# Kernel optimization log

Hardware: AMD Instinct MI355X
Metric: run time of the kernel (lower is better)

The kernel has to match this reference:

```python
import jax, jax.numpy as jnp
import numpy as np

B, N, S, C, H = 16, 64, 4096, 384, 6
DH = C // H
SCALE = DH ** -0.5


def setup_inputs() -> dict:
    k0 = jax.random.key(0)
    ks = jax.random.split(k0, 7)
    std = C ** -0.5
    return {
        "query": jax.random.normal(ks[0], (B, N, C), jnp.float32),
        "key": jax.random.normal(ks[1], (B, S, C), jnp.float32),
        "Wq": jax.random.normal(ks[2], (C, C), jnp.float32) * std,
        "Wk": jax.random.normal(ks[3], (C, C), jnp.float32) * std,
        "Wv": jax.random.normal(ks[4], (C, C), jnp.float32) * std,
        "Wp": jax.random.normal(ks[5], (C, C), jnp.float32) * std,
        "bp": jnp.zeros((C,), jnp.float32),
    }


def reference(query, key, Wq, Wk, Wv, Wp, bp):
    # q/k/v projections (no bias, matching qkv_bias=False); nn.Linear is x @ W.T
    q = (query @ Wq.T).reshape(B, N, H, DH).transpose(0, 2, 1, 3)  # [B,H,N,DH]
    k = (key @ Wk.T).reshape(B, S, H, DH).transpose(0, 2, 1, 3)    # [B,H,S,DH]
    v = (key @ Wv.T).reshape(B, S, H, DH).transpose(0, 2, 1, 3)    # [B,H,S,DH]

    attn = jnp.einsum('bhnd,bhsd->bhns', q, k) * SCALE  # [B,H,N,S]

    # hard_softmax over dim=-2 (the group/query axis): each key token is
    # hard-assigned (straight-through) to its argmax group.
    y_soft = jax.nn.softmax(attn, axis=-2)
    idx = jnp.argmax(y_soft, axis=-2)  # [B,H,S]
    y_hard = (jnp.arange(N)[:, None] == idx[..., None, :]).astype(attn.dtype)  # [B,H,N,S]
    a = y_hard + y_soft - jax.lax.stop_gradient(y_soft)

    # inv_attn renormalization over the key axis
    a = a / (a.sum(axis=-1, keepdims=True) + 1.0)

    out = jnp.einsum('bhns,bhsd->bhnd', a, v)            # [B,H,N,DH]
    out = out.transpose(0, 2, 1, 3).reshape(B, N, C)     # [B,N,C]
    return out @ Wp.T + bp
```

## Files before the change

### kernel.cpp

```cpp
#include <hip/hip_runtime.h>
#include <hip/hip_bf16.h>
#include <stdint.h>

#define B_ 16
#define N_ 64
#define S_ 4096
#define C_ 384
#define H_ 6
#define DH_ 64
#define SCALE_ 0.125f
#define TAU_ 2e-4f
#define LISTCAP 262144

typedef __attribute__((ext_vector_type(8))) short bf16x8;
typedef __attribute__((ext_vector_type(4))) float f32x4;

static __device__ __forceinline__ unsigned short f2bf(float x) {
    union { float f; unsigned u; } v; v.f = x;
    unsigned r = v.u + 0x7FFFu + ((v.u >> 16) & 1u);
    return (unsigned short)(r >> 16);
}
static __device__ __forceinline__ float bf2f(unsigned short b) {
    union { unsigned u; float f; } v; v.u = ((unsigned)b) << 16; return v.f;
}
static __device__ __forceinline__ float bfu_lo(unsigned u) {
    union { unsigned u; float f; } v; v.u = u << 16; return v.f;
}
static __device__ __forceinline__ float bfu_hi(unsigned u) {
    union { unsigned u; float f; } v; v.u = u & 0xFFFF0000u; return v.f;
}

static __device__ __forceinline__ void gl_lds16(const void* g, void* l) {
    __builtin_amdgcn_global_load_lds(
        (const __attribute__((address_space(1))) unsigned int*)g,
        (__attribute__((address_space(3))) unsigned int*)l, 16, 0, 0);
}

#define PREP_BLOCKS 8192
#define QK_BLOCKS   (8 * H_ * B_)

__global__ __launch_bounds__(384) void prepqk_kernel(const float* __restrict__ key,
                                                     unsigned short* __restrict__ khi,
                                                     unsigned short* __restrict__ klo,
                                                     const float* __restrict__ query,
                                                     const float* __restrict__ Wq,
                                                     const float* __restrict__ Wk,
                                                     float* __restrict__ qk,
                                                     unsigned short* __restrict__ qkhi,
                                                     unsigned short* __restrict__ qklo) {
    if (blockIdx.x < PREP_BLOCKS) {
        size_t gid = (size_t)blockIdx.x * 384 + threadIdx.x;
        size_t base = gid * 8;
        float4 x0 = *(const float4*)(key + base);
        float4 x1 = *(const float4*)(key + base + 4);
        float xs[8] = { x0.x, x0.y, x0.z, x0.w, x1.x, x1.y, x1.z, x1.w };
        unsigned short hi[8], lo[8];
#pragma unroll
        for (int i = 0; i < 8; ++i) {
            hi[i] = f2bf(xs[i]);
            lo[i] = f2bf(xs[i] - bf2f(hi[i]));
        }
        *(bf16x8*)(khi + base) = *(bf16x8*)hi;
        *(bf16x8*)(klo + base) = *(bf16x8*)lo;
        return;
    }
    __shared__ float qstage[8][C_];
    __shared__ float qv[8][DH_];
    int e = blockIdx.x - PREP_BLOCKS;
    int ng = e & 7;
    int h = (e >> 3) % H_;
    int b = e / (8 * H_);
    int t = threadIdx.x;
    int n0 = ng * 8;
#pragma unroll
    for (int i = 0; i < 8; ++i)
        qstage[i][t] = query[((size_t)(b * N_ + n0 + i)) * C_ + t];
    __syncthreads();
    if (t < 256) {
        int i0 = t >> 6, d = t & 63;
        const float4* wq = (const float4*)(Wq + (size_t)(h * DH_ + d) * C_);
        float accA = 0.f, accB = 0.f;
#pragma unroll 4
        for (int c4 = 0; c4 < C_ / 4; ++c4) {
            float4 w = wq[c4];
            float4 qa = *(const float4*)&qstage[i0][c4 * 4];
            float4 qb = *(const float4*)&qstage[i0 + 4][c4 * 4];
            accA += qa.x * w.x + qa.y * w.y + qa.z * w.z + qa.w * w.w;
            accB += qb.x * w.x + qb.y * w.y + qb.z * w.z + qb.w * w.w;
        }
        qv[i0][d] = accA * SCALE_;
        qv[i0 + 4][d] = accB * SCALE_;
    }
    __syncthreads();
    float a[8];
#pragma unroll
    for (int i = 0; i < 8; ++i) a[i] = 0.f;
    {
        const float* wk = Wk + (size_t)h * DH_ * C_ + t;
#pragma unroll 4
        for (int d = 0; d < DH_; ++d) {
            float w = wk[(size_t)d * C_];
#pragma unroll
            for (int i = 0; i < 8; ++i) a[i] += qv[i][d] * w;
        }
    }
#pragma unroll
    for (int i = 0; i < 8; ++i) qstage[i][t] = a[i];
    __syncthreads();
    {
        int r = t / 48, c0 = (t % 48) * 8;
        float v[8];
#pragma unroll
        for (int j = 0; j < 8; ++j) v[j] = qstage[r][c0 + j];
        unsigned short hi[8], lo[8];
#pragma unroll
        for (int j = 0; j < 8; ++j) {
            hi[j] = f2bf(v[j]);
            lo[j] = f2bf(v[j] - bf2f(hi[j]));
        }
        size_t o = ((size_t)(b * H_ + h) * N_ + n0 + r) * C_ + c0;
        float4 f0 = { v[0], v[1], v[2], v[3] };
        float4 f1 = { v[4], v[5], v[6], v[7] };
        *(float4*)(qk + o) = f0;
        *(float4*)(qk + o + 4) = f1;
        *(bf16x8*)(qkhi + o) = *(bf16x8*)hi;
        *(bf16x8*)(qklo + o) = *(bf16x8*)lo;
    }
}

__global__ __launch_bounds__(256) void attn_kernel(const unsigned short* __restrict__ qkhi,
                                                   const unsigned short* __restrict__ qklo,
                                                   const unsigned short* __restrict__ khi,
                                                   const unsigned short* __restrict__ klo,
                                                   unsigned int* __restrict__ idx,
                                                   unsigned int* __restrict__ flag_cnt,
                                                   unsigned int* __restrict__ flag_list) {
    __shared__ __align__(16) unsigned short sAhi[64 * 32];
    __shared__ __align__(16) unsigned short sAlo[64 * 32];
    __shared__ __align__(16) unsigned short sBhi[128 * 32];
    __shared__ __align__(16) unsigned short sBlo[128 * 32];
    int tid = threadIdx.x;
    int w = tid >> 6, l = tid & 63;
    int wm = w >> 1, wn = w & 1;
    int q4 = l >> 4, lm = l & 15;
    int s0 = blockIdx.x * 128;
    int h = blockIdx.y, b = blockIdx.z;
    size_t kbK = ((size_t)b * S_ + s0) * C_;
    size_t kbA = (size_t)(b * H_ + h) * N_ * C_;
    int trow16 = l >> 2;
    int tquart = ((l & 3) ^ ((l >> 3) & 3)) * 8;
    int sw = (q4 ^ ((lm >> 1) & 3)) * 8;

    f32x4 acc[2][4];
#pragma unroll
    for (int tm = 0; tm < 2; ++tm)
#pragma unroll
        for (int nt = 0; nt < 4; ++nt) acc[tm][nt] = (f32x4)0.f;

    for (int kc = 0; kc < C_; kc += 32) {
        __syncthreads();
#pragma unroll
        for (int i = 0; i < 6; ++i) {
            int gid = w * 6 + i;
            if (gid < 8) {
                gl_lds16(khi + kbK + (size_t)(gid * 16 + trow16) * C_ + kc + tquart,
                         (char*)sBhi + gid * 1024);
            } else if (gid < 16) {
                int g2 = gid - 8;
                gl_lds16(klo + kbK + (size_t)(g2 * 16 + trow16) * C_ + kc + tquart,
                         (char*)sBlo + g2 * 1024);
            } else if (gid < 20) {
                int g2 = gid - 16;
                gl_lds16(qkhi + kbA + (size_t)(g2 * 16 + trow16) * C_ + kc + tquart,
                         (char*)sAhi + g2 * 1024);
            } else {
                int g2 = gid - 20;
                gl_lds16(qklo + kbA + (size_t)(g2 * 16 + trow16) * C_ + kc + tquart,
                         (char*)sAlo + g2 * 1024);
            }
        }
        __syncthreads();
        bf16x8 ah[2], al[2];
#pragma unroll
        for (int tm = 0; tm < 2; ++tm) {
            int ar = (wm * 32 + tm * 16 + lm) * 32 + sw;
            ah[tm] = *(const bf16x8*)&sAhi[ar];
            al[tm] = *(const bf16x8*)&sAlo[ar];
        }
#pragma unroll
        for (int nt = 0; nt < 4; ++nt) {
            int nr = ((wn * 4 + nt) * 16 + lm) * 32 + sw;
            bf16x8 bh = *(const bf16x8*)&sBhi[nr];
            bf16x8 bl = *(const bf16x8*)&sBlo[nr];
#pragma unroll
            for (int tm = 0; tm < 2; ++tm) {
                acc[tm][nt] = __builtin_amdgcn_mfma_f32_16x16x32_bf16(ah[tm], bh, acc[tm][nt], 0, 0, 0);
                acc[tm][nt] = __builtin_amdgcn_mfma_f32_16x16x32_bf16(ah[tm], bl, acc[tm][nt], 0, 0, 0);
                acc[tm][nt] = __builtin_amdgcn_mfma_f32_16x16x32_bf16(al[tm], bh, acc[tm][nt], 0, 0, 0);
            }
        }
    }
    __syncthreads();

    float* rm1 = (float*)sBhi;
    float* rm2 = rm1 + 256;
    int* ri1 = (int*)(rm2 + 256);
    int* ri2 = ri1 + 256;

#pragma unroll
    for (int nt = 0; nt < 4; ++nt) {
        float m1 = -3.4e38f, m2 = -3.4e38f; int i1 = 0, i2 = 0;
#pragma unroll
        for (int tm = 0; tm < 2; ++tm)
#pragma unroll
            for (int r = 0; r < 4; ++r) {
                float v = acc[tm][nt][r];
                int row = wm * 32 + tm * 16 + q4 * 4 + r;
                if (v > m1) { m2 = m1; i2 = i1; m1 = v; i1 = row; }
                else if (v > m2) { m2 = v; i2 = row; }
            }
#pragma unroll
        for (int off = 16; off < 64; off <<= 1) {
            float om1 = __shfl_xor(m1, off), om2 = __shfl_xor(m2, off);
            int oi1 = __shfl_xor(i1, off), oi2 = __shfl_xor(i2, off);
            bool take = (om1 > m1) || (om1 == m1 && oi1 < i1);
            float w1 = take ? om1 : m1; int wi1 = take ? oi1 : i1;
            float l1 = take ? m1 : om1; int li1 = take ? i1 : oi1;
            float s2 = m2; int si2 = i2;
            if (om2 > s2) { s2 = om2; si2 = oi2; }
            if (l1 > s2) { s2 = l1; si2 = li1; }
            m1 = w1; i1 = wi1; m2 = s2; i2 = si2;
        }
        if (q4 == 0) {
            int cw = (wn * 4 + nt) * 16 + lm;
            rm1[wm * 128 + cw] = m1; rm2[wm * 128 + cw] = m2;
            ri1[wm * 128 + cw] = i1; ri2[wm * 128 + cw] = i2;
        }
    }
    __syncthreads();
    if (tid < 128) {
        float a1 = rm1[tid], a2 = rm2[tid];
        int ai1 = ri1[tid], ai2 = ri2[tid];
        float b1 = rm1[128 + tid], b2 = rm2[128 + tid];
        int bi1 = ri1[128 + tid], bi2 = ri2[128 + tid];
        float w1, s2; int wi1, wi2;
        if (b1 > a1) { w1 = b1; wi1 = bi1; s2 = a1; wi2 = ai1; if (b2 > s2) { s2 = b2; wi2 = bi2; } }
        else         { w1 = a1; wi1 = ai1; s2 = a2; wi2 = ai2; if (b1 > s2) { s2 = b1; wi2 = bi1; } }
        idx[(size_t)(b * H_ + h) * S_ + s0 + tid] = (unsigned)wi1;
        if (w1 - s2 < TAU_) {
            unsigned p = atomicAdd(flag_cnt, 1u);
            if (p < LISTCAP) {
                unsigned tok = (unsigned)((b * H_ + h) * S_ + s0 + tid);
                flag_list[p] = tok | ((unsigned)wi1 << 19) | ((unsigned)wi2 << 25);
            }
        }
    }
}

__global__ __launch_bounds__(256) void fixup_kernel(const float* __restrict__ qk,
                                                    const float* __restrict__ key,
                                                    const unsigned int* __restrict__ flag_list,
                                                    const unsigned int* __restrict__ flag_cnt,
                                                    unsigned int* __restrict__ idx) {
    int w = threadIdx.x >> 6, l = threadIdx.x & 63;
    unsigned total = flag_cnt[0];
    if (total > LISTCAP) total = LISTCAP;
    for (unsigned t = blockIdx.x * 4 + w; t < total; t += gridDim.x * 4) {
        unsigned e = flag_list[t];
        unsigned tok = e & 0x7FFFFu;
        int i1 = (int)((e >> 19) & 63u), i2 = (int)((e >> 25) & 63u);
        unsigned bh = tok >> 12;
        unsigned s = tok & 4095u;
        unsigned bb = bh / H_;
        int l32 = l & 31;
        const float* qrow = qk + ((size_t)bh * N_ + (l < 32 ? i1 : i2)) * C_ + l32 * 12;
        const float* krow = key + ((size_t)bb * S_ + s) * C_ + l32 * 12;
        float sum = 0.f;
#pragma unroll
        for (int c = 0; c < 12; ++c) sum += qrow[c] * krow[c];
#pragma unroll
        for (int off = 1; off < 32; off <<= 1) sum += __shfl_xor(sum, off);
        float d1 = __shfl(sum, 0);
        float d2 = __shfl(sum, 32);
        int win = (d2 > d1 || (d2 == d1 && i2 < i1)) ? i2 : i1;
        if (l == 0) idx[(size_t)bh * S_ + s] = (unsigned)win;
    }
}

__global__ __launch_bounds__(256) void hist_build_kernel(const unsigned int* __restrict__ idx,
                                                         unsigned int* __restrict__ offs,
                                                         unsigned int* __restrict__ order) {
    __shared__ unsigned int cnts[N_];
    __shared__ unsigned int pos[N_];
    int tid = threadIdx.x;
    int bh = blockIdx.x;
    if (tid < N_) cnts[tid] = 0u;
    __syncthreads();
    const unsigned int* idxp = idx + (size_t)bh * S_;
    for (int s = tid; s < S_; s += 256) atomicAdd(&cnts[idxp[s]], 1u);
    __syncthreads();
    if (tid < N_) {
        unsigned v = cnts[tid];
        unsigned x = v;
#pragma unroll
        for (int off = 1; off < 64; off <<= 1) {
            unsigned y = __shfl_up(x, off);
            if (tid >= off) x += y;
        }
        unsigned excl = x - v;
        pos[tid] = excl;
        offs[(size_t)bh * 65 + tid] = excl;
        if (tid == 63) offs[(size_t)bh * 65 + 64] = x;
    }
    __syncthreads();
    unsigned int* op = order + (size_t)bh * S_;
    for (int s = tid; s < S_; s += 256) {
        unsigned g = idxp[s];
        unsigned p = atomicAdd(&pos[g], 1u);
        op[p] = (unsigned)s;
    }
}

#define AGG_PARTS 8
__global__ __launch_bounds__(512) void aggv_kernel(const unsigned short* __restrict__ khi,
                                                   const unsigned int* __restrict__ order,
                                                   const unsigned int* __restrict__ offs,
                                                   const float* __restrict__ Wv,
                                                   float* __restrict__ gvn) {
    __shared__ float lrows[AGG_PARTS][C_];
    int tid = threadIdx.x;
    int part = tid >> 6, l = tid & 63;
    int h = blockIdx.y, b = blockIdx.z;
    int bh = b * H_ + h;
    int g = blockIdx.x;
    unsigned beg = offs[(size_t)bh * 65 + g];
    unsigned end = offs[(size_t)bh * 65 + g + 1];
    int cnt = (int)(end - beg);
    float inv = 1.f / ((float)cnt + 1.f);
    const unsigned int* op = order + (size_t)bh * S_ + beg;
    const unsigned int* kbase = (const unsigned int*)(khi + (size_t)b * S_ * C_);
    float a0 = 0.f, a1 = 0.f, a2 = 0.f, a3 = 0.f, a4 = 0.f, a5 = 0.f;
    for (int base = part * 64; base < cnt; base += 64 * AGG_PARTS) {
        int m = cnt - base; if (m > 64) m = 64;
        unsigned sv = (l < m) ? op[base + l] : 0u;
        int i = 0;
        for (; i + 8 <= m; i += 8) {
            int ss[8];
#pragma unroll
            for (int j = 0; j < 8; ++j) ss[j] = __shfl((int)sv, i + j);
            unsigned u[8][3];
#pragma unroll
            for (int j = 0; j < 8; ++j) {
                const unsigned int* kp = kbase + (size_t)ss[j] * (C_ / 2) + l * 3;
                u[j][0] = kp[0]; u[j][1] = kp[1]; u[j][2] = kp[2];
            }
#pragma unroll
            for (int j = 0; j < 8; ++j) {
                a0 += bfu_lo(u[j][0]); a1 += bfu_hi(u[j][0]);
                a2 += bfu_lo(u[j][1]); a3 += bfu_hi(u[j][1]);
                a4 += bfu_lo(u[j][2]); a5 += bfu_hi(u[j][2]);
            }
        }
        for (; i < m; ++i) {
            int s = (int)__shfl((int)sv, i);
            const unsigned int* kp = kbase + (size_t)s * (C_ / 2) + l * 3;
            unsigned u0 = kp[0], u1 = kp[1], u2 = kp[2];
            a0 += bfu_lo(u0); a1 += bfu_hi(u0);
            a2 += bfu_lo(u1); a3 += bfu_hi(u1);
            a4 += bfu_lo(u2); a5 += bfu_hi(u2);
        }
    }
    float* lp = &lrows[part][l * 6];
    lp[0] = a0 * inv; lp[1] = a1 * inv; lp[2] = a2 * inv;
    lp[3] = a3 * inv; lp[4] = a4 * inv; lp[5] = a5 * inv;
    __syncthreads();
    if (part == 0) {
        const float* wrow = Wv + (size_t)(h * DH_ + l) * C_;
        float acc = 0.f;
#pragma unroll 4
        for (int c4 = 0; c4 < C_ / 4; ++c4) {
            float4 z = *(const float4*)&lrows[0][c4 * 4];
#pragma unroll
            for (int p = 1; p < AGG_PARTS; ++p) {
                float4 y = *(const float4*)&lrows[p][c4 * 4];
                z.x += y.x; z.y += y.y; z.z += y.z; z.w += y.w;
            }
            float4 wv = *(const float4*)&wrow[c4 * 4];
            acc += z.x * wv.x + z.y * wv.y + z.z * wv.z + z.w * wv.w;
        }
        gvn[((size_t)bh * N_ + g) * DH_ + l] = acc;
    }
}

__global__ __launch_bounds__(384) void out_kernel(const float* __restrict__ gvn,
                                                  const float* __restrict__ Wp,
                                                  const float* __restrict__ bp,
                                                  float* __restrict__ out) {
    __shared__ float vals[4][C_];
    int blk = blockIdx.x;
    int b = blk >> 4, n0 = (blk & 15) * 4;
    int t = threadIdx.x;
    int h = t >> 6, d = t & 63;
#pragma unroll
    for (int j = 0; j < 4; ++j)
        vals[j][t] = gvn[((size_t)(b * H_ + h) * N_ + n0 + j) * DH_ + d];
    __syncthreads();
    const float4* w4 = (const float4*)(Wp + (size_t)t * C_);
    float s0 = bp[t], s1 = s0, s2 = s0, s3 = s0;
    const float4* v0 = (const float4*)vals[0];
    const float4* v1 = (const float4*)vals[1];
    const float4* v2 = (const float4*)vals[2];
    const float4* v3 = (const float4*)vals[3];
#pragma unroll 4
    for (int i = 0; i < C_ / 4; ++i) {
        float4 w = w4[i];
        float4 a0 = v0[i]; s0 += a0.x * w.x + a0.y * w.y + a0.z * w.z + a0.w * w.w;
        float4 a1 = v1[i]; s1 += a1.x * w.x + a1.y * w.y + a1.z * w.z + a1.w * w.w;
        float4 a2 = v2[i]; s2 += a2.x * w.x + a2.y * w.y + a2.z * w.z + a2.w * w.w;
        float4 a3 = v3[i]; s3 += a3.x * w.x + a3.y * w.y + a3.z * w.z + a3.w * w.w;
    }
    size_t ob = ((size_t)b * N_ + n0) * C_ + t;
    out[ob] = s0;
    out[ob + C_] = s1;
    out[ob + 2 * C_] = s2;
    out[ob + 3 * C_] = s3;
}

extern "C" void kernel_launch(void* const* d_in, const int* in_sizes, int n_in,
                              void* d_out, int out_size, void* d_ws, size_t ws_size,
                              hipStream_t stream) {
    (void)in_sizes; (void)n_in; (void)out_size; (void)ws_size;
    const float* query = (const float*)d_in[0];
    const float* key   = (const float*)d_in[1];
    const float* Wq    = (const float*)d_in[2];
    const float* Wk    = (const float*)d_in[3];
    const float* Wv    = (const float*)d_in[4];
    const float* Wp    = (const float*)d_in[5];
    const float* bp    = (const float*)d_in[6];
    float* out = (float*)d_out;

    char* ws = (char*)d_ws;
    size_t off = 0;
    unsigned short* khi  = (unsigned short*)(ws + off); off += (size_t)B_ * S_ * C_ * 2;
    unsigned short* klo  = (unsigned short*)(ws + off); off += (size_t)B_ * S_ * C_ * 2;
    float* qk            = (float*)(ws + off);          off += (size_t)B_ * H_ * N_ * C_ * 4;
    unsigned short* qkhi = (unsigned short*)(ws + off); off += (size_t)B_ * H_ * N_ * C_ * 2;
    unsigned short* qklo = (unsigned short*)(ws + off); off += (size_t)B_ * H_ * N_ * C_ * 2;
    unsigned int* idx    = (unsigned int*)(ws + off);   off += (size_t)B_ * H_ * S_ * 4;
    unsigned int* order  = (unsigned int*)(ws + off);   off += (size_t)B_ * H_ * S_ * 4;
    unsigned int* offs   = (unsigned int*)(ws + off);   off += (size_t)B_ * H_ * 65 * 4;
    float* gvn           = (float*)(ws + off);          off += (size_t)B_ * H_ * N_ * DH_ * 4;
    unsigned int* fcnt   = (unsigned int*)(ws + off);   off += 256;
    unsigned int* flist  = (unsigned int*)(ws + off);   off += (size_t)LISTCAP * 4;

    hipMemsetAsync(fcnt, 0, 256, stream);

    prepqk_kernel<<<PREP_BLOCKS + QK_BLOCKS, 384, 0, stream>>>(key, khi, klo,
                                                               query, Wq, Wk, qk, qkhi, qklo);
    attn_kernel<<<dim3(S_ / 128, H_, B_), 256, 0, stream>>>(qkhi, qklo, khi, klo, idx, fcnt, flist);
    fixup_kernel<<<256, 256, 0, stream>>>(qk, key, flist, fcnt, idx);
    hist_build_kernel<<<B_ * H_, 256, 0, stream>>>(idx, offs, order);
    aggv_kernel<<<dim3(N_, H_, B_), 512, 0, stream>>>(khi, order, offs, Wv, gvn);
    out_kernel<<<B_ * N_ / 4, 384, 0, stream>>>(gvn, Wp, bp, out);
}
```

Measured before the change: 449.9 us.

## Transpose Wp/Wv in prep kernel for coalesced weight reads in aggv and out

Adds extra blocks to the prep kernel that transpose Wp and Wv into workspace, so the aggv and out kernels read weights with coalesced column access instead of per-thread strided rows. aggv now reduces partial rows once into shared memory and splits the Wv matvec across all 8 parts. out_kernel runs one block per output row instead of four rows per block. The key bf16 split is also changed to 4-wide accesses. The cost is extra transpose work and writes on every call, plus more blocks and syncs.

```diff
diff --git a/kernel.cpp b/kernel.cpp
--- a/kernel.cpp
+++ b/kernel.cpp
@@ -14,6 +14,7 @@
 
 typedef __attribute__((ext_vector_type(8))) short bf16x8;
 typedef __attribute__((ext_vector_type(4))) float f32x4;
+typedef __attribute__((ext_vector_type(4))) unsigned short u16x4;
 
 static __device__ __forceinline__ unsigned short f2bf(float x) {
     union { float f; unsigned u; } v; v.f = x;
@@ -38,6 +39,7 @@
 
 #define PREP_BLOCKS 8192
 #define QK_BLOCKS   (8 * H_ * B_)
+#define TR_BLOCKS   72
 
 __global__ __launch_bounds__(384) void prepqk_kernel(const float* __restrict__ key,
                                                      unsigned short* __restrict__ khi,
@@ -47,30 +49,62 @@
                                                      const float* __restrict__ Wk,
                                                      float* __restrict__ qk,
                                                      unsigned short* __restrict__ qkhi,
-                                                     unsigned short* __restrict__ qklo) {
-    if (blockIdx.x < PREP_BLOCKS) {
-        size_t gid = (size_t)blockIdx.x * 384 + threadIdx.x;
-        size_t base = gid * 8;
-        float4 x0 = *(const float4*)(key + base);
-        float4 x1 = *(const float4*)(key + base + 4);
-        float xs[8] = { x0.x, x0.y, x0.z, x0.w, x1.x, x1.y, x1.z, x1.w };
-        unsigned short hi[8], lo[8];
-#pragma unroll
-        for (int i = 0; i < 8; ++i) {
-            hi[i] = f2bf(xs[i]);
-            lo[i] = f2bf(xs[i] - bf2f(hi[i]));
-        }
-        *(bf16x8*)(khi + base) = *(bf16x8*)hi;
-        *(bf16x8*)(klo + base) = *(bf16x8*)lo;
-        return;
-    }
+                                                     unsigned short* __restrict__ qklo,
+                                                     const float* __restrict__ Wp,
+                                                     const float* __restrict__ Wv,
+                                                     float* __restrict__ wpT,
+                                                     float* __restrict__ wvT) {
     __shared__ float qstage[8][C_];
     __shared__ float qv[8][DH_];
+    __shared__ float trt[64][65];
+    int t = threadIdx.x;
+    if (blockIdx.x < PREP_BLOCKS) {
+        size_t blk = (size_t)blockIdx.x * 3072;
+#pragma unroll
+        for (int half = 0; half < 2; ++half) {
+            size_t base = blk + (size_t)half * 1536 + (size_t)t * 4;
+            float4 x = *(const float4*)(key + base);
+            float xs[4] = { x.x, x.y, x.z, x.w };
+            unsigned short hi[4], lo[4];
+#pragma unroll
+            for (int i = 0; i < 4; ++i) {
+                hi[i] = f2bf(xs[i]);
+                lo[i] = f2bf(xs[i] - bf2f(hi[i]));
+            }
+            *(u16x4*)(khi + base) = *(u16x4*)hi;
+            *(u16x4*)(klo + base) = *(u16x4*)lo;
+        }
+        return;
+    }
     int e = blockIdx.x - PREP_BLOCKS;
+    if (e >= QK_BLOCKS) {
+        int e2 = e - QK_BLOCKS;
+        const float* src = (e2 < 36) ? Wp : Wv;
+        float* dst = (e2 < 36) ? wpT : wvT;
+        int tile = e2 % 36;
+        int r0 = (tile / 6) * 64, c0 = (tile % 6) * 64;
+        if (t < 256) {
+#pragma unroll
+            for (int rep = 0; rep < 16; ++rep) {
+                int idx = rep * 256 + t;
+                int r = idx >> 6, c = idx & 63;
+                trt[r][c] = src[(size_t)(r0 + r) * C_ + c0 + c];
+            }
+        }
+        __syncthreads();
+        if (t < 256) {
+#pragma unroll
+            for (int rep = 0; rep < 16; ++rep) {
+                int idx = rep * 256 + t;
+                int rT = idx >> 6, cT = idx & 63;
+                dst[(size_t)(c0 + rT) * C_ + r0 + cT] = trt[cT][rT];
+            }
+        }
+        return;
+    }
     int ng = e & 7;
     int h = (e >> 3) % H_;
     int b = e / (8 * H_);
-    int t = threadIdx.x;
     int n0 = ng * 8;
 #pragma unroll
     for (int i = 0; i < 8; ++i)
@@ -325,9 +359,11 @@
 __global__ __launch_bounds__(512) void aggv_kernel(const unsigned short* __restrict__ khi,
                                                    const unsigned int* __restrict__ order,
                                                    const unsigned int* __restrict__ offs,
-                                                   const float* __restrict__ Wv,
+                                                   const float* __restrict__ wvT,
                                                    float* __restrict__ gvn) {
     __shared__ float lrows[AGG_PARTS][C_];
+    __shared__ float zrow[C_];
+    __shared__ float pacc[AGG_PARTS][DH_];
     int tid = threadIdx.x;
     int part = tid >> 6, l = tid & 63;
     int h = blockIdx.y, b = blockIdx.z;
@@ -374,56 +410,48 @@
     lp[0] = a0 * inv; lp[1] = a1 * inv; lp[2] = a2 * inv;
     lp[3] = a3 * inv; lp[4] = a4 * inv; lp[5] = a5 * inv;
     __syncthreads();
+    if (tid < C_) {
+        float z = lrows[0][tid];
+#pragma unroll
+        for (int p = 1; p < AGG_PARTS; ++p) z += lrows[p][tid];
+        zrow[tid] = z;
+    }
+    __syncthreads();
+    {
+        float a = 0.f;
+        int cb = part * (C_ / AGG_PARTS);
+#pragma unroll 8
+        for (int cc = 0; cc < C_ / AGG_PARTS; ++cc) {
+            int c = cb + cc;
+            a += zrow[c] * wvT[(size_t)c * C_ + h * DH_ + l];
+        }
+        pacc[part][l] = a;
+    }
+    __syncthreads();
     if (part == 0) {
-        const float* wrow = Wv + (size_t)(h * DH_ + l) * C_;
-        float acc = 0.f;
-#pragma unroll 4
-        for (int c4 = 0; c4 < C_ / 4; ++c4) {
-            float4 z = *(const float4*)&lrows[0][c4 * 4];
-#pragma unroll
-            for (int p = 1; p < AGG_PARTS; ++p) {
-                float4 y = *(const float4*)&lrows[p][c4 * 4];
-                z.x += y.x; z.y += y.y; z.z += y.z; z.w += y.w;
-            }
-            float4 wv = *(const float4*)&wrow[c4 * 4];
-            acc += z.x * wv.x + z.y * wv.y + z.z * wv.z + z.w * wv.w;
-        }
+        float acc = pacc[0][l];
+#pragma unroll
+        for (int p = 1; p < AGG_PARTS; ++p) acc += pacc[p][l];
         gvn[((size_t)bh * N_ + g) * DH_ + l] = acc;
     }
 }
 
 __global__ __launch_bounds__(384) void out_kernel(const float* __restrict__ gvn,
-                                                  const float* __restrict__ Wp,
+                                                  const float* __restrict__ wpT,
                                                   const float* __restrict__ bp,
                                                   float* __restrict__ out) {
-    __shared__ float vals[4][C_];
-    int blk = blockIdx.x;
-    int b = blk >> 4, n0 = (blk & 15) * 4;
+    __shared__ float vals[C_];
+    int bn = blockIdx.x;
+    int b = bn >> 6, n = bn & 63;
     int t = threadIdx.x;
     int h = t >> 6, d = t & 63;
-#pragma unroll
-    for (int j = 0; j < 4; ++j)
-        vals[j][t] = gvn[((size_t)(b * H_ + h) * N_ + n0 + j) * DH_ + d];
-    __syncthreads();
-    const float4* w4 = (const float4*)(Wp + (size_t)t * C_);
-    float s0 = bp[t], s1 = s0, s2 = s0, s3 = s0;
-    const float4* v0 = (const float4*)vals[0];
-    const float4* v1 = (const float4*)vals[1];
-    const float4* v2 = (const float4*)vals[2];
-    const float4* v3 = (const float4*)vals[3];
-#pragma unroll 4
-    for (int i = 0; i < C_ / 4; ++i) {
-        float4 w = w4[i];
-        float4 a0 = v0[i]; s0 += a0.x * w.x + a0.y * w.y + a0.z * w.z + a0.w * w.w;
-        float4 a1 = v1[i]; s1 += a1.x * w.x + a1.y * w.y + a1.z * w.z + a1.w * w.w;
-        float4 a2 = v2[i]; s2 += a2.x * w.x + a2.y * w.y + a2.z * w.z + a2.w * w.w;
-        float4 a3 = v3[i]; s3 += a3.x * w.x + a3.y * w.y + a3.z * w.z + a3.w * w.w;
-    }
-    size_t ob = ((size_t)b * N_ + n0) * C_ + t;
-    out[ob] = s0;
-    out[ob + C_] = s1;
-    out[ob + 2 * C_] = s2;
-    out[ob + 3 * C_] = s3;
+    vals[t] = gvn[((size_t)(b * H_ + h) * N_ + n) * DH_ + d];
+    __syncthreads();
+    float s = bp[t];
+#pragma unroll 8
+    for (int c = 0; c < C_; ++c)
+        s += vals[c] * wpT[(size_t)c * C_ + t];
+    out[(size_t)bn * C_ + t] = s;
 }
 
 extern "C" void kernel_launch(void* const* d_in, const int* in_sizes, int n_in,
@@ -450,16 +478,18 @@
     unsigned int* order  = (unsigned int*)(ws + off);   off += (size_t)B_ * H_ * S_ * 4;
     unsigned int* offs   = (unsigned int*)(ws + off);   off += (size_t)B_ * H_ * 65 * 4;
     float* gvn           = (float*)(ws + off);          off += (size_t)B_ * H_ * N_ * DH_ * 4;
+    float* wpT           = (float*)(ws + off);          off += (size_t)C_ * C_ * 4;
+    float* wvT           = (float*)(ws + off);          off += (size_t)C_ * C_ * 4;
     unsigned int* fcnt   = (unsigned int*)(ws + off);   off += 256;
     unsigned int* flist  = (unsigned int*)(ws + off);   off += (size_t)LISTCAP * 4;
 
     hipMemsetAsync(fcnt, 0, 256, stream);
 
-    prepqk_kernel<<<PREP_BLOCKS + QK_BLOCKS, 384, 0, stream>>>(key, khi, klo,
-                                                               query, Wq, Wk, qk, qkhi, qklo);
+    prepqk_kernel<<<PREP_BLOCKS + QK_BLOCKS + TR_BLOCKS, 384, 0, stream>>>(
+        key, khi, klo, query, Wq, Wk, qk, qkhi, qklo, Wp, Wv, wpT, wvT);
     attn_kernel<<<dim3(S_ / 128, H_, B_), 256, 0, stream>>>(qkhi, qklo, khi, klo, idx, fcnt, flist);
     fixup_kernel<<<256, 256, 0, stream>>>(qk, key, flist, fcnt, idx);
     hist_build_kernel<<<B_ * H_, 256, 0, stream>>>(idx, offs, order);
-    aggv_kernel<<<dim3(N_, H_, B_), 512, 0, stream>>>(khi, order, offs, Wv, gvn);
-    out_kernel<<<B_ * N_ / 4, 384, 0, stream>>>(gvn, Wp, bp, out);
-}
+    aggv_kernel<<<dim3(N_, H_, B_), 512, 0, stream>>>(khi, order, offs, wvT, gvn);
+    out_kernel<<<B_ * N_, 384, 0, stream>>>(gvn, wpT, bp, out);
+}
```

Result: faster. 402.3 us (-10.6%).
